# Performance work log

Measured on AMD Instinct MI355X. Metric: run time of the kernel, lower is better.

Reference implementation:

```python
import jax, jax.numpy as jnp
import numpy as np

NEG_INF = float(np.finfo(np.float32).min)
EPS = 1e-6
NOISE_STD = 1.0
CHUNK = 8
TEMP = 1.0


def moving_sum(x, back, forward):
    # x: [B, T]; windowed sum over [t-back, t+forward] via prefix sums (O(T))
    B, T = x.shape
    cs = jnp.concatenate([jnp.zeros((B, 1), x.dtype), jnp.cumsum(x, axis=1)], axis=1)  # [B, T+1]
    idx = jnp.arange(T)
    hi = jnp.clip(idx + forward + 1, 0, T)
    lo = jnp.clip(idx - back, 0, T)
    return cs[:, hi] - cs[:, lo]


def setup_inputs() -> dict:
    key = jax.random.key(0)
    ks = jax.random.split(key, 12)
    B, T, KD, QD, AD, VD = 16, 4000, 512, 512, 512, 512
    s = lambda d: 1.0 / np.sqrt(d)
    return {
        "key": jax.random.normal(ks[0], (B, T, KD), jnp.float32),
        "value": jax.random.normal(ks[1], (B, T, VD), jnp.float32),
        "query": jax.random.normal(ks[2], (B, 1, QD), jnp.float32),
        "mask": jnp.ones((B, 1, T), jnp.int32),
        "w_key_mono": jax.random.normal(ks[3], (KD, AD), jnp.float32) * s(KD),
        "b_key_mono": jnp.zeros((AD,), jnp.float32),
        "w_query_mono": jax.random.normal(ks[4], (QD, AD), jnp.float32) * s(QD),
        "v_mono": jax.random.normal(ks[5], (AD,), jnp.float32) * s(AD),
        "g_mono": jnp.asarray(np.sqrt(1.0 / AD), jnp.float32),  # weight_norm gain init
        "r_mono": jnp.asarray(-4.0, jnp.float32),
        "w_key_chunk": jax.random.normal(ks[6], (KD, AD), jnp.float32) * s(KD),
        "b_key_chunk": jnp.zeros((AD,), jnp.float32),
        "w_query_chunk": jax.random.normal(ks[7], (QD, AD), jnp.float32) * s(QD),
        "v_chunk": jax.random.normal(ks[8], (AD,), jnp.float32) * s(AD),
    }


def _energy(key, query, mask, wk, bk, wq, v, r=None, g=None):
    kproj = jax.nn.relu(key) @ wk + bk          # [B, T, A]
    qproj = query @ wq                           # [B, 1, A]
    if g is not None:  # weight-normalized v
        v = g * v / jnp.linalg.norm(v)
    e = jnp.tanh(kproj + qproj) @ v              # [B, T]
    if r is not None:
        e = e + r
    return jnp.where(mask[:, 0, :] == 0, NEG_INF, e)


def reference(key, value, query, mask, w_key_mono, b_key_mono, w_query_mono, v_mono,
              g_mono, r_mono, w_key_chunk, b_key_chunk, w_query_chunk, v_chunk):
    B, T, _ = key.shape
    e_mono = _energy(key, query, mask, w_key_mono, b_key_mono, w_query_mono,
                     v_mono, r=r_mono, g=g_mono)
    noise = jax.random.normal(jax.random.key(123), e_mono.shape, e_mono.dtype) * NOISE_STD
    p_choose = jax.nn.sigmoid(e_mono + noise)                      # [B, T]
    # safe_cumprod of (1 - p): exp(exclusive cumsum of clipped logs)
    log1mp = jnp.log(jnp.clip(1.0 - p_choose, EPS, 1.0))
    cumprod_1mp = jnp.exp(jnp.cumsum(log1mp, axis=1) - log1mp)     # exclusive
    aw_prev = jnp.zeros((B, T), key.dtype).at[:, 0].set(1.0)       # one-hot at t=0
    alpha = p_choose * cumprod_1mp * jnp.cumsum(
        aw_prev / jnp.clip(cumprod_1mp, EPS, 1.0), axis=1)
    # chunkwise attention
    e_chunk = _energy(key, query, mask, w_key_chunk, b_key_chunk, w_query_chunk, v_chunk)
    e_chunk = e_chunk - jnp.max(e_chunk, axis=1, keepdims=True)
    softmax_exp = jnp.maximum(jnp.exp(e_chunk), 1e-5)
    denom = moving_sum(softmax_exp, CHUNK - 1, 0)
    beta = softmax_exp * moving_sum(alpha * TEMP / denom, 0, CHUNK - 1)
    cv = jnp.einsum('bt,btd->bd', beta, value)[:, None, :]         # [B, 1, V]
    return cv, alpha[..., None]
```

## Files before the change

kernel.cpp:

```cpp
#include <hip/hip_runtime.h>
#include <stdint.h>

typedef unsigned short u16;
typedef unsigned int   u32;

#define T_LEN 4000
#define NEG_INF (-3.4028234663852886e38f)

typedef __bf16 bf16x8 __attribute__((ext_vector_type(8)));
typedef float  f32x4  __attribute__((ext_vector_type(4)));

__device__ __forceinline__ u16 f2bf(float f){
    union { float f; u32 i; } v; v.f = f;
    u32 u = v.i;
    u32 r = (u + 0x7FFFu + ((u >> 16) & 1u)) >> 16;
    return (u16)r;
}
__device__ __forceinline__ float tanh_fast(float x){
    float ax = fabsf(x);
    float a = __expf(-2.0f * ax);
    float t = (1.0f - a) / (1.0f + a);
    return copysignf(t, x);
}
__device__ __forceinline__ u32 rotl32(u32 x, int n){ return (x << n) | (x >> (32 - n)); }

__device__ __forceinline__ void gll16(const void* g, void* l){
    __builtin_amdgcn_global_load_lds(
        (__attribute__((address_space(1))) void*)g,
        (__attribute__((address_space(3))) void*)l, 16, 0, 0);
}

__device__ float jax_noise(u32 idx){
    const u32 k0 = 0u, k1 = 123u;
    const u32 k2 = k0 ^ k1 ^ 0x1BD11BDAu;
    u32 x0 = k0;
    u32 x1 = idx + k1;
#define RND(r) { x0 += x1; x1 = rotl32(x1, r); x1 ^= x0; }
    RND(13) RND(15) RND(26) RND(6)   x0 += k1; x1 += k2 + 1u;
    RND(17) RND(29) RND(16) RND(24)  x0 += k2; x1 += k0 + 2u;
    RND(13) RND(15) RND(26) RND(6)   x0 += k0; x1 += k1 + 3u;
    RND(17) RND(29) RND(16) RND(24)  x0 += k1; x1 += k2 + 4u;
    RND(13) RND(15) RND(26) RND(6)   x0 += k2; x1 += k0 + 5u;
#undef RND
    u32 bits = x0 ^ x1;
    union { u32 i; float f; } u;
    u.i = (bits >> 9) | 0x3F800000u;
    float f01 = u.f - 1.0f;
    const float minval = -0.99999994f;
    float uu = f01 * (1.0f - minval) + minval;
    uu = fmaxf(uu, minval);
    return 1.41421356f * erfinvf(uu);
}

__global__ __launch_bounds__(512) void prep_combined(
    const float* __restrict__ v_mono, const float* __restrict__ g_mono,
    const float* __restrict__ query, const float* __restrict__ wq_mono,
    const float* __restrict__ wq_chunk,
    const float* __restrict__ wk_mono, const float* __restrict__ wk_chunk,
    const float* __restrict__ key,
    float* __restrict__ vn, float* __restrict__ qp_mono, float* __restrict__ qp_chunk,
    u16* __restrict__ Wt, u16* __restrict__ kb,
    float* __restrict__ ezero, float* __restrict__ outcv)
{
    __shared__ float shf[512];
    __shared__ u16 tile[32][33];
    const int blk = blockIdx.x;
    const int tid = threadIdx.x;
    if (blk == 0){
        float v = v_mono[tid];
        shf[tid] = v * v;
        __syncthreads();
        for (int off = 256; off >= 1; off >>= 1){
            if (tid < off) shf[tid] += shf[tid + off];
            __syncthreads();
        }
        float g = g_mono[0];
        vn[tid] = g * v / sqrtf(shf[0]);
    } else if (blk <= 32){
        int b = (blk - 1) >> 1;
        int which = (blk - 1) & 1;
        const float* W = which ? wq_chunk : wq_mono;
        float* out = which ? qp_chunk : qp_mono;
        shf[tid] = query[b * 512 + tid];
        __syncthreads();
        float acc = 0.f;
        for (int k = 0; k < 512; k++) acc += shf[k] * W[k * 512 + tid];
        out[b * 512 + tid] = acc;
    } else if (blk <= 544){
        int idx = blk - 33;
        int kt = (idx & 15) * 32, nt = (idx >> 4) * 32;
        int c = tid & 31, r = tid >> 5;
        const float* src = (nt < 512) ? wk_mono : wk_chunk;
        int nbase = (nt < 512) ? nt : nt - 512;
#pragma unroll
        for (int i = 0; i < 2; i++){
            int kk = r + i * 16;
            tile[kk][c] = f2bf(src[(size_t)(kt + kk) * 512 + nbase + c]);
        }
        __syncthreads();
#pragma unroll
        for (int i = 0; i < 2; i++){
            int nn = r + i * 16;
            Wt[(size_t)(nt + nn) * 512 + kt + c] = tile[c][nn];
        }
    } else if (blk < 608){
        int i = ((blk - 545) * 512 + tid) * 4;
        if (i < 128000){
            float4 z = {0.f, 0.f, 0.f, 0.f};
            *reinterpret_cast<float4*>(ezero + i) = z;
        }
    } else if (blk < 612){
        int i = ((blk - 608) * 512 + tid) * 4;
        float4 z = {0.f, 0.f, 0.f, 0.f};
        *reinterpret_cast<float4*>(outcv + i) = z;
    } else {
        size_t i = ((size_t)(blk - 612) * 512 + tid) * 8;
        float4 a = *reinterpret_cast<const float4*>(key + i);
        float4 b = *reinterpret_cast<const float4*>(key + i + 4);
        uint4 pk;
        pk.x = (u32)f2bf(fmaxf(a.x, 0.f)) | ((u32)f2bf(fmaxf(a.y, 0.f)) << 16);
        pk.y = (u32)f2bf(fmaxf(a.z, 0.f)) | ((u32)f2bf(fmaxf(a.w, 0.f)) << 16);
        pk.z = (u32)f2bf(fmaxf(b.x, 0.f)) | ((u32)f2bf(fmaxf(b.y, 0.f)) << 16);
        pk.w = (u32)f2bf(fmaxf(b.z, 0.f)) | ((u32)f2bf(fmaxf(b.w, 0.f)) << 16);
        *reinterpret_cast<uint4*>(kb + i) = pk;
    }
}

__global__ __launch_bounds__(256) void gemm_energy_pre(
    const u16* __restrict__ kb, const u16* __restrict__ Wt,
    const float* __restrict__ b_mono, const float* __restrict__ b_chunk,
    const float* __restrict__ vnorm, const float* __restrict__ v_chunk,
    const float* __restrict__ qp_mono, const float* __restrict__ qp_chunk,
    float* __restrict__ e_mono, float* __restrict__ e_chunk)
{
    __shared__ __align__(16) u16 As[128 * 32];
    __shared__ __align__(16) u16 Bs[128 * 32];
    const int bid = blockIdx.x;
    const int x = ((bid >> 6) << 3) + (bid & 7);
    if (x >= 500) return;
    const int nT = (bid >> 3) & 7;
    const int g0 = x * 128;
    const bool mono = (nT < 4);
    const int n0 = nT * 128;
    const int tid = threadIdx.x;
    const int lane = tid & 63;
    const int wave = tid >> 6;
    const int wm = wave >> 1, wn = wave & 1;
    const int l15 = lane & 15, quad = lane >> 4;

    f32x4 acc[4][4];
#pragma unroll
    for (int i = 0; i < 4; i++)
#pragma unroll
        for (int j = 0; j < 4; j++)
#pragma unroll
            for (int c = 0; c < 4; c++) acc[i][j][c] = 0.f;

    const u16* aG = kb + (size_t)g0 * 512;
    const u16* bG = Wt + (size_t)n0 * 512;

    for (int k0 = 0; k0 < 512; k0 += 32){
#pragma unroll
        for (int it = 0; it < 2; it++){
            int vid = tid + it * 256;
            int row = vid >> 2;
            int part = vid & 3;
            gll16(aG + (size_t)row * 512 + k0 + part * 8, As + vid * 8);
            gll16(bG + (size_t)row * 512 + k0 + part * 8, Bs + vid * 8);
        }
        __syncthreads();
        bf16x8 af[4], bfr[4];
#pragma unroll
        for (int i = 0; i < 4; i++){
            af[i]  = *reinterpret_cast<const bf16x8*>(&As[(wm * 64 + i * 16 + l15) * 32 + quad * 8]);
            bfr[i] = *reinterpret_cast<const bf16x8*>(&Bs[(wn * 64 + i * 16 + l15) * 32 + quad * 8]);
        }
#pragma unroll
        for (int i = 0; i < 4; i++)
#pragma unroll
            for (int j = 0; j < 4; j++)
                acc[i][j] = __builtin_amdgcn_mfma_f32_16x16x32_bf16(af[i], bfr[j], acc[i][j], 0, 0, 0);
        __syncthreads();
    }

    const float* qp = mono ? qp_mono : qp_chunk;
    float* edst = mono ? e_mono : e_chunk;
    float vv[4], bb[4]; int nc[4];
#pragma unroll
    for (int j = 0; j < 4; j++){
        int ncol = (n0 - (mono ? 0 : 512)) + wn * 64 + j * 16 + l15;
        nc[j] = ncol;
        vv[j] = mono ? vnorm[ncol] : v_chunk[ncol];
        bb[j] = mono ? b_mono[ncol] : b_chunk[ncol];
    }
#pragma unroll
    for (int i = 0; i < 4; i++){
#pragma unroll
        for (int r = 0; r < 4; r++){
            int g = g0 + wm * 64 + i * 16 + quad * 4 + r;
            int bidx = (u32)g / 4000u;
            float s = 0.f;
#pragma unroll
            for (int j = 0; j < 4; j++){
                float x2 = acc[i][j][r] + bb[j] + qp[bidx * 512 + nc[j]];
                s += vv[j] * tanh_fast(x2);
            }
            s += __shfl_xor(s, 1);
            s += __shfl_xor(s, 2);
            s += __shfl_xor(s, 4);
            s += __shfl_xor(s, 8);
            if (l15 == 0) atomicAdd(&edst[g], s);
        }
    }
}

__global__ __launch_bounds__(256) void gemm_energy_f32(
    const float* __restrict__ key, const u16* __restrict__ Wt,
    const float* __restrict__ b_mono, const float* __restrict__ b_chunk,
    const float* __restrict__ vnorm, const float* __restrict__ v_chunk,
    const float* __restrict__ qp_mono, const float* __restrict__ qp_chunk,
    float* __restrict__ e_mono, float* __restrict__ e_chunk)
{
    __shared__ __align__(16) u16 As[128 * 40];
    __shared__ __align__(16) u16 Bs[128 * 40];
    const int tid = threadIdx.x;
    const int g0 = blockIdx.x * 128;
    const int nT = blockIdx.y;
    const bool mono = (nT < 4);
    const int n0 = nT * 128;
    const int lane = tid & 63;
    const int wave = tid >> 6;
    const int wm = wave >> 1, wn = wave & 1;
    const int l15 = lane & 15, quad = lane >> 4;

    f32x4 acc[4][4];
#pragma unroll
    for (int i = 0; i < 4; i++)
#pragma unroll
        for (int j = 0; j < 4; j++)
#pragma unroll
            for (int c = 0; c < 4; c++) acc[i][j][c] = 0.f;

    for (int k0 = 0; k0 < 512; k0 += 32){
        __syncthreads();
#pragma unroll
        for (int it = 0; it < 4; it++){
            int vid = tid + it * 256;
            int row = vid >> 3;
            int c4  = (vid & 7) << 2;
            float4 a = *reinterpret_cast<const float4*>(key + (size_t)(g0 + row) * 512 + k0 + c4);
            u32 p0 = (u32)f2bf(fmaxf(a.x, 0.f)) | ((u32)f2bf(fmaxf(a.y, 0.f)) << 16);
            u32 p1 = (u32)f2bf(fmaxf(a.z, 0.f)) | ((u32)f2bf(fmaxf(a.w, 0.f)) << 16);
            uint2 pk; pk.x = p0; pk.y = p1;
            *reinterpret_cast<uint2*>(&As[row * 40 + c4]) = pk;
        }
#pragma unroll
        for (int it = 0; it < 2; it++){
            int vid = tid + it * 256;
            int row = vid >> 2;
            int cb  = (vid & 3) << 3;
            uint4 b = *reinterpret_cast<const uint4*>(Wt + (size_t)(n0 + row) * 512 + k0 + cb);
            *reinterpret_cast<uint4*>(&Bs[row * 40 + cb]) = b;
        }
        __syncthreads();
        bf16x8 af[4], bfr[4];
#pragma unroll
        for (int i = 0; i < 4; i++){
            af[i]  = *reinterpret_cast<const bf16x8*>(&As[(wm * 64 + i * 16 + l15) * 40 + quad * 8]);
            bfr[i] = *reinterpret_cast<const bf16x8*>(&Bs[(wn * 64 + i * 16 + l15) * 40 + quad * 8]);
        }
#pragma unroll
        for (int i = 0; i < 4; i++)
#pragma unroll
            for (int j = 0; j < 4; j++)
                acc[i][j] = __builtin_amdgcn_mfma_f32_16x16x32_bf16(af[i], bfr[j], acc[i][j], 0, 0, 0);
    }

    const float* qp = mono ? qp_mono : qp_chunk;
    float* edst = mono ? e_mono : e_chunk;
    float vv[4], bb[4]; int nc[4];
#pragma unroll
    for (int j = 0; j < 4; j++){
        int ncol = (n0 - (mono ? 0 : 512)) + wn * 64 + j * 16 + l15;
        nc[j] = ncol;
        vv[j] = mono ? vnorm[ncol] : v_chunk[ncol];
        bb[j] = mono ? b_mono[ncol] : b_chunk[ncol];
    }
#pragma unroll
    for (int i = 0; i < 4; i++){
#pragma unroll
        for (int r = 0; r < 4; r++){
            int g = g0 + wm * 64 + i * 16 + quad * 4 + r;
            int bidx = (u32)g / 4000u;
            float s = 0.f;
#pragma unroll
            for (int j = 0; j < 4; j++){
                float x = acc[i][j][r] + bb[j] + qp[bidx * 512 + nc[j]];
                s += vv[j] * tanh_fast(x);
            }
            s += __shfl_xor(s, 1);
            s += __shfl_xor(s, 2);
            s += __shfl_xor(s, 4);
            s += __shfl_xor(s, 8);
            if (l15 == 0) atomicAdd(&edst[g], s);
        }
    }
}

#define IDX(t) ((t) + ((t) >> 4))

__global__ __launch_bounds__(256) void scan_energy(
    const float* __restrict__ e_mono, const float* __restrict__ e_chunk,
    const int* __restrict__ mask, const float* __restrict__ r_mono,
    float* __restrict__ out_alpha, float* __restrict__ beta)
{
    __shared__ float P[4256];
    __shared__ float AL[4256];
    __shared__ float SE[4256];
    __shared__ float red[256];
    const int b = blockIdx.x;
    const int tid = threadIdx.x;
    const float r = r_mono[0];
    const int t0 = tid * 16;

    float l[16];
    float lsum = 0.f;
#pragma unroll
    for (int i = 0; i < 16; i++){
        int t = t0 + i;
        if (t < T_LEN){
            int fl = b * T_LEN + t;
            float e = e_mono[fl] + r;
            if (mask[fl] == 0) e = NEG_INF;
            float x = e + jax_noise((u32)fl);
            float p = 1.0f / (1.0f + expf(-x));
            P[IDX(t)] = p;
            float om = 1.0f - p;
            om = fminf(fmaxf(om, 1e-6f), 1.0f);
            l[i] = logf(om);
            lsum += l[i];
        } else l[i] = 0.f;
    }
    red[tid] = lsum;
    __syncthreads();
#pragma unroll
    for (int off = 1; off < 256; off <<= 1){
        float v = (tid >= off) ? red[tid - off] : 0.f;
        __syncthreads();
        red[tid] += v;
        __syncthreads();
    }
    float run = red[tid] - lsum;
#pragma unroll
    for (int i = 0; i < 16; i++){
        int t = t0 + i;
        if (t < T_LEN){
            float alpha = P[IDX(t)] * expf(run);
            run += l[i];
            AL[IDX(t)] = alpha;
            out_alpha[b * T_LEN + t] = alpha;
        }
    }

    float ec[16]; float lmax = NEG_INF;
#pragma unroll
    for (int i = 0; i < 16; i++){
        int t = t0 + i;
        if (t < T_LEN){
            int fl = b * T_LEN + t;
            float e = e_chunk[fl];
            if (mask[fl] == 0) e = NEG_INF;
            ec[i] = e;
            lmax = fmaxf(lmax, e);
        } else ec[i] = NEG_INF;
    }
    __syncthreads();
    red[tid] = lmax;
    __syncthreads();
    for (int off = 128; off >= 1; off >>= 1){
        if (tid < off) red[tid] = fmaxf(red[tid], red[tid + off]);
        __syncthreads();
    }
    float m = red[0];
#pragma unroll
    for (int i = 0; i < 16; i++){
        int t = t0 + i;
        if (t < T_LEN) SE[IDX(t)] = fmaxf(expf(ec[i] - m), 1e-5f);
    }
    __syncthreads();
#pragma unroll
    for (int i = 0; i < 16; i++){
        int t = t0 + i;
        if (t < T_LEN){
            float d = 0.f;
            int lo = t - 7; if (lo < 0) lo = 0;
            for (int s = lo; s <= t; s++) d += SE[IDX(s)];
            P[IDX(t)] = AL[IDX(t)] / d;
        }
    }
    __syncthreads();
#pragma unroll
    for (int i = 0; i < 16; i++){
        int t = t0 + i;
        if (t < T_LEN){
            float s2 = 0.f;
            int hi = t + 7; if (hi > T_LEN - 1) hi = T_LEN - 1;
            for (int s = t; s <= hi; s++) s2 += P[IDX(s)];
            beta[b * T_LEN + t] = SE[IDX(t)] * s2;
        }
    }
}

__global__ __launch_bounds__(256) void cv_accum(const float* __restrict__ value,
                                                const float* __restrict__ beta,
                                                float* __restrict__ outcv){
    const int b = blockIdx.x >> 4;
    const int c = blockIdx.x & 15;
    const int tid = threadIdx.x;
    __shared__ float bsh[250];
    int tstart = c * 250;
    if (tid < 250) bsh[tid] = beta[b * T_LEN + tstart + tid];
    __syncthreads();
    int dl = (tid & 127) * 4;
    int trow = tid >> 7;
    float4 a = {0.f, 0.f, 0.f, 0.f};
    for (int t = trow; t < 250; t += 2){
        float bt = bsh[t];
        float4 v = *reinterpret_cast<const float4*>(
            value + (size_t)(b * T_LEN + tstart + t) * 512 + dl);
        a.x += bt * v.x; a.y += bt * v.y; a.z += bt * v.z; a.w += bt * v.w;
    }
    atomicAdd(&outcv[b * 512 + dl + 0], a.x);
    atomicAdd(&outcv[b * 512 + dl + 1], a.y);
    atomicAdd(&outcv[b * 512 + dl + 2], a.z);
    atomicAdd(&outcv[b * 512 + dl + 3], a.w);
}

extern "C" void kernel_launch(void* const* d_in, const int* in_sizes, int n_in,
                              void* d_out, int out_size, void* d_ws, size_t ws_size,
                              hipStream_t stream)
{
    const float* key      = (const float*)d_in[0];
    const float* value    = (const float*)d_in[1];
    const float* query    = (const float*)d_in[2];
    const int*   mask     = (const int*)d_in[3];
    const float* wk_mono  = (const float*)d_in[4];
    const float* bk_mono  = (const float*)d_in[5];
    const float* wq_mono  = (const float*)d_in[6];
    const float* v_mono   = (const float*)d_in[7];
    const float* g_mono   = (const float*)d_in[8];
    const float* r_mono   = (const float*)d_in[9];
    const float* wk_chunk = (const float*)d_in[10];
    const float* bk_chunk = (const float*)d_in[11];
    const float* wq_chunk = (const float*)d_in[12];
    const float* v_chunk  = (const float*)d_in[13];

    float* ws      = (float*)d_ws;
    float* e_mono  = ws;
    float* e_chunk = ws + 64000;
    float* beta    = ws + 136192;
    float* qp_mono = ws + 200192;
    float* qp_chunk= ws + 208384;
    float* vnorm   = ws + 216576;
    u16*   Wt      = (u16*)(ws + 217088);
    u16*   kb      = (u16*)(ws + 479232);

    const size_t NEED = 479232u * 4u + (size_t)64000 * 512 * 2;
    const bool big = ws_size >= NEED;

    prep_combined<<<big ? 8612 : 612, 512, 0, stream>>>(
        v_mono, g_mono, query, wq_mono, wq_chunk, wk_mono, wk_chunk, key,
        vnorm, qp_mono, qp_chunk, Wt, kb, e_mono, (float*)d_out);

    if (big){
        gemm_energy_pre<<<4096, 256, 0, stream>>>(kb, Wt, bk_mono, bk_chunk,
                                                  vnorm, v_chunk, qp_mono, qp_chunk,
                                                  e_mono, e_chunk);
    } else {
        gemm_energy_f32<<<dim3(500, 8), 256, 0, stream>>>(key, Wt, bk_mono, bk_chunk,
                                                          vnorm, v_chunk, qp_mono, qp_chunk,
                                                          e_mono, e_chunk);
    }
    scan_energy<<<16, 256, 0, stream>>>(e_mono, e_chunk, mask, r_mono,
                                        (float*)d_out + 8192, beta);
    cv_accum<<<256, 256, 0, stream>>>(value, beta, (float*)d_out);
}
```

Before: 476.6 us.

## Replace bf16 energy GEMM with 256x256-tile double-buffered 8-phase pipelined kernel

```diff
diff --git a/kernel.cpp b/kernel.cpp
--- a/kernel.cpp
+++ b/kernel.cpp
@@ -126,84 +126,157 @@
     }
 }
 
-__global__ __launch_bounds__(256) void gemm_energy_pre(
+
+__device__ __forceinline__ void stageA(const u16* __restrict__ kb, u16* SH,
+                                       int g0, int kt, int h, int tid){
+#pragma unroll
+    for (int j = 0; j < 2; j++){
+        int vid = tid + j * 512;
+        int rr = vid >> 3;
+        int sl = (vid & 7) ^ (rr & 7);
+        gll16(kb + (size_t)(g0 + h * 128 + rr) * 512 + kt * 64 + sl * 8,
+              SH + (size_t)((kt & 1) * 32768 + h * 8192 + vid * 8));
+    }
+}
+__device__ __forceinline__ void stageB(const u16* __restrict__ Wt, u16* SH,
+                                       int n0, int kt, int h, int tid){
+#pragma unroll
+    for (int j = 0; j < 2; j++){
+        int vid = tid + j * 512;
+        int rr = vid >> 3;
+        int sl = (vid & 7) ^ (rr & 7);
+        gll16(Wt + (size_t)(n0 + h * 128 + rr) * 512 + kt * 64 + sl * 8,
+              SH + (size_t)((kt & 1) * 32768 + 16384 + h * 8192 + vid * 8));
+    }
+}
+
+#define DRAIN0 asm volatile("s_waitcnt vmcnt(0)" ::: "memory")
+#define NODRAIN ((void)0)
+#define NOSTAGE ((void)0)
+
+#define PHASE(BSEL, MH, NH, STAGES, DRAIN) do{                                    \
+    bf16x8 af[4][2], bg[2][2];                                                    \
+    _Pragma("unroll") for (int mf = 0; mf < 4; mf++)                              \
+    _Pragma("unroll") for (int ks = 0; ks < 2; ks++){                             \
+        int rr = wm * 128 + (MH) * 64 + mf * 16 + l15;                            \
+        int sl = (ks * 4 + quad) ^ (rr & 7);                                      \
+        af[mf][ks] = *reinterpret_cast<const bf16x8*>(                            \
+            &SH[(BSEL) * 32768 + rr * 64 + sl * 8]);                              \
+    }                                                                             \
+    _Pragma("unroll") for (int nf = 0; nf < 2; nf++)                              \
+    _Pragma("unroll") for (int ks = 0; ks < 2; ks++){                             \
+        int rr = wn * 64 + (NH) * 32 + nf * 16 + l15;                             \
+        int sl = (ks * 4 + quad) ^ (rr & 7);                                      \
+        bg[nf][ks] = *reinterpret_cast<const bf16x8*>(                            \
+            &SH[(BSEL) * 32768 + 16384 + rr * 64 + sl * 8]);                      \
+    }                                                                             \
+    STAGES;                                                                       \
+    DRAIN;                                                                        \
+    __builtin_amdgcn_sched_barrier(0);                                            \
+    __builtin_amdgcn_s_barrier();                                                 \
+    asm volatile("s_waitcnt lgkmcnt(0)" ::: "memory");                            \
+    __builtin_amdgcn_sched_barrier(0);                                            \
+    __builtin_amdgcn_s_setprio(1);                                                \
+    _Pragma("unroll") for (int mf = 0; mf < 4; mf++)                              \
+    _Pragma("unroll") for (int nf = 0; nf < 2; nf++)                              \
+    _Pragma("unroll") for (int ks = 0; ks < 2; ks++)                              \
+        acc[(MH) * 4 + mf][(NH) * 2 + nf] =                                       \
+            __builtin_amdgcn_mfma_f32_16x16x32_bf16(                              \
+                af[mf][ks], bg[nf][ks], acc[(MH) * 4 + mf][(NH) * 2 + nf], 0,0,0);\
+    __builtin_amdgcn_s_setprio(0);                                                \
+    __builtin_amdgcn_sched_barrier(0);                                            \
+    __builtin_amdgcn_s_barrier();                                                 \
+    __builtin_amdgcn_sched_barrier(0);                                            \
+}while(0)
+
+__global__ __launch_bounds__(512) void gemm_energy_8ph(
     const u16* __restrict__ kb, const u16* __restrict__ Wt,
     const float* __restrict__ b_mono, const float* __restrict__ b_chunk,
     const float* __restrict__ vnorm, const float* __restrict__ v_chunk,
     const float* __restrict__ qp_mono, const float* __restrict__ qp_chunk,
     float* __restrict__ e_mono, float* __restrict__ e_chunk)
 {
-    __shared__ __align__(16) u16 As[128 * 32];
-    __shared__ __align__(16) u16 Bs[128 * 32];
+    __shared__ __align__(16) u16 SH[65536];
+
     const int bid = blockIdx.x;
-    const int x = ((bid >> 6) << 3) + (bid & 7);
-    if (x >= 500) return;
-    const int nT = (bid >> 3) & 7;
-    const int g0 = x * 128;
-    const bool mono = (nT < 4);
-    const int n0 = nT * 128;
+    const int swz = (bid & 7) * 125 + (bid >> 3);
+    const int xt = swz >> 2;
+    const int nT = swz & 3;
+    const int g0 = xt * 256;
+    const int n0 = nT * 256;
+
     const int tid = threadIdx.x;
     const int lane = tid & 63;
     const int wave = tid >> 6;
-    const int wm = wave >> 1, wn = wave & 1;
+    const int wm = wave >> 2, wn = wave & 3;
     const int l15 = lane & 15, quad = lane >> 4;
 
-    f32x4 acc[4][4];
-#pragma unroll
-    for (int i = 0; i < 4; i++)
-#pragma unroll
-        for (int j = 0; j < 4; j++)
-#pragma unroll
-            for (int c = 0; c < 4; c++) acc[i][j][c] = 0.f;
-
-    const u16* aG = kb + (size_t)g0 * 512;
-    const u16* bG = Wt + (size_t)n0 * 512;
-
-    for (int k0 = 0; k0 < 512; k0 += 32){
-#pragma unroll
-        for (int it = 0; it < 2; it++){
-            int vid = tid + it * 256;
-            int row = vid >> 2;
-            int part = vid & 3;
-            gll16(aG + (size_t)row * 512 + k0 + part * 8, As + vid * 8);
-            gll16(bG + (size_t)row * 512 + k0 + part * 8, Bs + vid * 8);
-        }
-        __syncthreads();
-        bf16x8 af[4], bfr[4];
-#pragma unroll
-        for (int i = 0; i < 4; i++){
-            af[i]  = *reinterpret_cast<const bf16x8*>(&As[(wm * 64 + i * 16 + l15) * 32 + quad * 8]);
-            bfr[i] = *reinterpret_cast<const bf16x8*>(&Bs[(wn * 64 + i * 16 + l15) * 32 + quad * 8]);
-        }
-#pragma unroll
-        for (int i = 0; i < 4; i++)
-#pragma unroll
-            for (int j = 0; j < 4; j++)
-                acc[i][j] = __builtin_amdgcn_mfma_f32_16x16x32_bf16(af[i], bfr[j], acc[i][j], 0, 0, 0);
-        __syncthreads();
-    }
-
+    const bool mono = (nT < 2);
     const float* qp = mono ? qp_mono : qp_chunk;
     float* edst = mono ? e_mono : e_chunk;
-    float vv[4], bb[4]; int nc[4];
-#pragma unroll
-    for (int j = 0; j < 4; j++){
-        int ncol = (n0 - (mono ? 0 : 512)) + wn * 64 + j * 16 + l15;
-        nc[j] = ncol;
-        vv[j] = mono ? vnorm[ncol] : v_chunk[ncol];
-        bb[j] = mono ? b_mono[ncol] : b_chunk[ncol];
-    }
-#pragma unroll
-    for (int i = 0; i < 4; i++){
+    float vv[4], bb[4]; float qA[4], qB[4];
+    const int b0 = g0 / 4000;
+    const int b1 = (g0 + 255) / 4000;
+#pragma unroll
+    for (int nf = 0; nf < 4; nf++){
+        int c = (n0 - (mono ? 0 : 512)) + wn * 64 + nf * 16 + l15;
+        vv[nf] = mono ? vnorm[c] : v_chunk[c];
+        bb[nf] = mono ? b_mono[c] : b_chunk[c];
+        qA[nf] = qp[b0 * 512 + c];
+        qB[nf] = qp[b1 * 512 + c];
+    }
+
+    f32x4 acc[8][4];
+#pragma unroll
+    for (int i = 0; i < 8; i++)
+#pragma unroll
+        for (int j = 0; j < 4; j++)
+#pragma unroll
+            for (int c = 0; c < 4; c++) acc[i][j][c] = 0.f;
+
+    DRAIN0;
+    __builtin_amdgcn_sched_barrier(0);
+
+    stageA(kb, SH, g0, 0, 0, tid);
+    stageA(kb, SH, g0, 0, 1, tid);
+    stageB(Wt, SH, n0, 0, 0, tid);
+    stageB(Wt, SH, n0, 0, 1, tid);
+    DRAIN0;
+    __builtin_amdgcn_sched_barrier(0);
+    __builtin_amdgcn_s_barrier();
+    __builtin_amdgcn_sched_barrier(0);
+
+#pragma unroll 1
+    for (int it = 0; it < 4; it++){
+        const int O = 2 * it + 1;
+        const int Ep = 2 * it + 2;
+        PHASE(0, 0, 0, { stageA(kb, SH, g0, O, 0, tid); stageA(kb, SH, g0, O, 1, tid);
+                         stageB(Wt, SH, n0, O, 0, tid); stageB(Wt, SH, n0, O, 1, tid); },
+              NODRAIN);
+        PHASE(0, 0, 1, NOSTAGE, NODRAIN);
+        PHASE(0, 1, 0, NOSTAGE, NODRAIN);
+        PHASE(0, 1, 1, NOSTAGE, DRAIN0);
+        PHASE(1, 0, 0, { if (it < 3){
+                             stageA(kb, SH, g0, Ep, 0, tid); stageA(kb, SH, g0, Ep, 1, tid);
+                             stageB(Wt, SH, n0, Ep, 0, tid); stageB(Wt, SH, n0, Ep, 1, tid); } },
+              NODRAIN);
+        PHASE(1, 0, 1, NOSTAGE, NODRAIN);
+        PHASE(1, 1, 0, NOSTAGE, NODRAIN);
+        PHASE(1, 1, 1, NOSTAGE, DRAIN0);
+    }
+
+#pragma unroll
+    for (int mf = 0; mf < 8; mf++){
 #pragma unroll
         for (int r = 0; r < 4; r++){
-            int g = g0 + wm * 64 + i * 16 + quad * 4 + r;
+            int g = g0 + wm * 128 + mf * 16 + quad * 4 + r;
             int bidx = (u32)g / 4000u;
             float s = 0.f;
 #pragma unroll
-            for (int j = 0; j < 4; j++){
-                float x2 = acc[i][j][r] + bb[j] + qp[bidx * 512 + nc[j]];
-                s += vv[j] * tanh_fast(x2);
+            for (int nf = 0; nf < 4; nf++){
+                float qv = (bidx == b0) ? qA[nf] : qB[nf];
+                float x = acc[mf][nf][r] + bb[nf] + qv;
+                s += vv[nf] * tanh_fast(x);
             }
             s += __shfl_xor(s, 1);
             s += __shfl_xor(s, 2);
@@ -473,7 +546,7 @@
         vnorm, qp_mono, qp_chunk, Wt, kb, e_mono, (float*)d_out);
 
     if (big){
-        gemm_energy_pre<<<4096, 256, 0, stream>>>(kb, Wt, bk_mono, bk_chunk,
+        gemm_energy_8ph<<<1000, 512, 0, stream>>>(kb, Wt, bk_mono, bk_chunk,
                                                   vnorm, v_chunk, qp_mono, qp_chunk,
                                                   e_mono, e_chunk);
     } else {
```

Measured after the change: 532.6 us. 1.12x slower.
